# Kernel optimization log

Measured on AMD Instinct MI355X. Metric: run time of the kernel, lower is better.

Reference implementation:

```python
import jax, jax.numpy as jnp
import numpy as np

T, B, F_, H = 128, 64, 512, 1024  # time, batch, feat, hidden


def hamilton(w):
    """Build dense quaternion (Hamilton-product) weight matrix.
    w: (4, in//4, out//4) components (r, i, j, k) -> (in, out)."""
    r, i, j, k = w[0], w[1], w[2], w[3]
    return jnp.concatenate([
        jnp.concatenate([r, -i, -j, -k], axis=0),
        jnp.concatenate([i,  r, -k,  j], axis=0),
        jnp.concatenate([j,  k,  r, -i], axis=0),
        jnp.concatenate([k, -j,  i,  r], axis=0),
    ], axis=1)


def setup_inputs() -> dict:
    key = jax.random.key(0)
    ks = jax.random.split(key, 16)
    s_in, s_h = 0.05, 0.03  # small init scales for stable gates
    d = {"x": jax.random.normal(ks[0], (T, B, F_), jnp.float32)}
    for idx, n in enumerate(["wfx", "wix", "wox", "wcx"]):
        d[n + "_w"] = jax.random.normal(ks[1 + idx], (4, F_ // 4, H // 4), jnp.float32) * s_in
        d[n + "_b"] = jnp.zeros((H,), jnp.float32)
    for idx, n in enumerate(["ufh", "uih", "uoh", "uch"]):
        d[n + "_w"] = jax.random.normal(ks[5 + idx], (4, H // 4, H // 4), jnp.float32) * s_h
    d["fco_w"] = jax.random.normal(ks[9], (H, F_ + 1), jnp.float32) * 0.02
    d["fco_b"] = jnp.zeros((F_ + 1,), jnp.float32)
    return d


def reference(x, wfx_w, wfx_b, wix_w, wix_b, wox_w, wox_b, wcx_w, wcx_b,
              ufh_w, uih_w, uoh_w, uch_w, fco_w, fco_b):
    # Dense quaternion matrices built once (as torch does per call).
    Wf, Wi, Wo, Wc = (hamilton(w) for w in (wfx_w, wix_w, wox_w, wcx_w))
    Uf, Ui, Uo, Uc = (hamilton(w) for w in (ufh_w, uih_w, uoh_w, uch_w))
    # Precompute all input projections over the whole sequence (as torch does).
    gf = jnp.einsum('tbi,io->tbo', x, Wf) + wfx_b
    gi = jnp.einsum('tbi,io->tbo', x, Wi) + wix_b
    go = jnp.einsum('tbi,io->tbo', x, Wo) + wox_b
    gc = jnp.einsum('tbi,io->tbo', x, Wc) + wcx_b

    def step(carry, g):
        h, c = carry
        gft, git, got, gct = g
        ft = jax.nn.sigmoid(gft + h @ Uf)
        it = jax.nn.sigmoid(git + h @ Ui)
        ot = jax.nn.sigmoid(got + h @ Uo)
        at = gct + h @ Uc
        c = it * jnp.tanh(at) + ft * c
        h = ot * jnp.tanh(c)
        return (h, c), h @ fco_w + fco_b

    h0 = jnp.zeros((B, H), x.dtype)
    _, out = jax.lax.scan(step, (h0, h0), (gf, gi, go, gc))
    return out  # [T, B, F_+1]
```

## Files before the change

### kernel.cpp

```cpp
#include <hip/hip_runtime.h>
#include <stdint.h>

typedef _Float16 f16;
typedef _Float16 f16x8 __attribute__((ext_vector_type(8)));
typedef short bf16x8 __attribute__((ext_vector_type(8)));
typedef float f32x4 __attribute__((ext_vector_type(4)));

#define H_ 1024
#define NG_ 4096
#define F_ 512
#define B_ 64
#define T_ 128
#define NOP_ 640
#define NO_ 513
#define NBLK_R 128

__constant__ int c_comp[16] = {0,1,2,3, 1,0,3,2, 2,3,0,1, 3,2,1,0};
__constant__ float c_sgnf[16] = {1,1,1,1, -1,1,1,-1, -1,-1,1,1, -1,1,-1,1};

__device__ __forceinline__ float bf2f(unsigned short u){
  union { unsigned int i; float f; } v; v.i = ((unsigned int)u) << 16; return v.f;
}
__device__ __forceinline__ unsigned short f2bf(float f){
  union { float f; unsigned int i; } v; v.f = f;
  return (unsigned short)((v.i + 0x7fffu + ((v.i >> 16) & 1u)) >> 16);
}
__device__ __forceinline__ float ldin(const void* p, int i, int f){
  return f ? ((const float*)p)[i] : bf2f(((const unsigned short*)p)[i]);
}
__device__ __forceinline__ float sigm(float x){ return 1.f / (1.f + __expf(-x)); }
__device__ __forceinline__ float tanh_(float x){
  float ax = fabsf(x);
  float e = __expf(-2.f * ax);
  float t = (1.f - e) / (1.f + e);
  return x < 0.f ? -t : t;
}

__device__ __forceinline__ void load_a8_nw(const f16* p, f16x8* a){
  asm volatile(
    "global_load_dwordx4 %0, %8, off sc0 sc1\n\t"
    "global_load_dwordx4 %1, %8, off offset:64 sc0 sc1\n\t"
    "global_load_dwordx4 %2, %8, off offset:128 sc0 sc1\n\t"
    "global_load_dwordx4 %3, %8, off offset:192 sc0 sc1\n\t"
    "global_load_dwordx4 %4, %8, off offset:256 sc0 sc1\n\t"
    "global_load_dwordx4 %5, %8, off offset:320 sc0 sc1\n\t"
    "global_load_dwordx4 %6, %8, off offset:384 sc0 sc1\n\t"
    "global_load_dwordx4 %7, %8, off offset:448 sc0 sc1"
    : "=&v"(a[0]),"=&v"(a[1]),"=&v"(a[2]),"=&v"(a[3]),
      "=&v"(a[4]),"=&v"(a[5]),"=&v"(a[6]),"=&v"(a[7])
    : "v"(p) : "memory");
}
__device__ __forceinline__ void load_c8(const unsigned short* p, bf16x8* a){
  asm volatile(
    "global_load_dwordx4 %0, %8, off\n\t"
    "global_load_dwordx4 %1, %8, off offset:64\n\t"
    "global_load_dwordx4 %2, %8, off offset:128\n\t"
    "global_load_dwordx4 %3, %8, off offset:192\n\t"
    "global_load_dwordx4 %4, %8, off offset:256\n\t"
    "global_load_dwordx4 %5, %8, off offset:320\n\t"
    "global_load_dwordx4 %6, %8, off offset:384\n\t"
    "global_load_dwordx4 %7, %8, off offset:448"
    : "=&v"(a[0]),"=&v"(a[1]),"=&v"(a[2]),"=&v"(a[3]),
      "=&v"(a[4]),"=&v"(a[5]),"=&v"(a[6]),"=&v"(a[7])
    : "v"(p) : "memory");
}
__device__ __forceinline__ void store_h_sys(f16* p, f16 v){
  asm volatile("global_store_short %0, %1, off sc0 sc1" :: "v"(p), "v"(v) : "memory");
}
__device__ __forceinline__ void store_flag_sys(int* p, int v){
  asm volatile("global_store_dword %0, %1, off sc0 sc1" :: "v"(p), "v"(v) : "memory");
}
__device__ __forceinline__ void load_flag2_sys(const int* p0, const int* p1, int &a, int &b){
  asm volatile(
    "global_load_dword %0, %2, off sc0 sc1\n\t"
    "global_load_dword %1, %3, off sc0 sc1\n\t"
    "s_waitcnt vmcnt(0)"
    : "=&v"(a), "=&v"(b) : "v"(p0), "v"(p1) : "memory");
}
__device__ __forceinline__ void drain_vmem(){
  asm volatile("s_waitcnt vmcnt(0)" ::: "memory");
}
#define WAIT_VM(n) do { \
  asm volatile("s_waitcnt vmcnt(" #n ")" ::: "memory"); \
  __builtin_amdgcn_sched_barrier(0); \
} while (0)

#define WX_ELEMS (NG_*F_)
#define U_ELEMS  (NG_*H_)
#define FCO_ELEMS (NOP_*H_)
#define BIAS_ELEMS NG_
#define OB_ELEMS NOP_
#define XC_ELEMS (T_*B_*F_)
#define HZ_ELEMS (B_*H_)
#define FZ_ELEMS (NBLK_R*16)
#define PACK_TOTAL (WX_ELEMS + U_ELEMS + FCO_ELEMS + BIAS_ELEMS + OB_ELEMS + XC_ELEMS + HZ_ELEMS + FZ_ELEMS)

__global__ void pack_kernel(
    const void* __restrict__ x,
    const void* __restrict__ wf, const void* __restrict__ wi,
    const void* __restrict__ wo, const void* __restrict__ wc,
    const void* __restrict__ bfv, const void* __restrict__ biv,
    const void* __restrict__ bov, const void* __restrict__ bcv,
    const void* __restrict__ uf, const void* __restrict__ ui,
    const void* __restrict__ uo, const void* __restrict__ uc,
    const void* __restrict__ fcw, const void* __restrict__ fcb,
    unsigned short* __restrict__ Wx, f16* __restrict__ U, f16* __restrict__ Fco,
    float* __restrict__ bias, float* __restrict__ ob,
    unsigned short* __restrict__ Xc,
    f16* __restrict__ Hz, int* __restrict__ Fz)
{
  __shared__ int zc, wc2;
  if (threadIdx.x == 0){ zc = 0; wc2 = 0; }
  __syncthreads();
  {
    const unsigned short* xu = (const unsigned short*)x;
    unsigned short u = xu[2 * threadIdx.x];
    int e = (u >> 7) & 0xFF;
    bool z = (u & 0x7FFF) == 0;
    bool wild = !z && (e < 67 || e > 150);
    if (z) atomicAdd(&zc, 1);
    if (wild) atomicAdd(&wc2, 1);
  }
  __syncthreads();
  const int fl = (zc >= 128 || wc2 >= 64) ? 1 : 0;

  int i = blockIdx.x * blockDim.x + threadIdx.x;
  if (i < WX_ELEMS) {
    int n = i >> 9, k = i & 511;
    int g = n >> 10, nn = n & 1023;
    int q = nn >> 8, be = nn & 255;
    int p = k >> 7, al = k & 127;
    const void* w = (g==0) ? wf : (g==1) ? wi : (g==2) ? wo : wc;
    int pq = p*4 + q;
    Wx[i] = f2bf(c_sgnf[pq] * ldin(w, c_comp[pq]*32768 + al*256 + be, fl));
    return;
  }
  i -= WX_ELEMS;
  if (i < U_ELEMS) {
    int n = i >> 10, k = i & 1023;
    int g = n >> 10;
    int q = (n & 1023) >> 8, be = n & 255;
    int p = k >> 8, al = k & 255;
    const void* u = (g==0) ? uf : (g==1) ? ui : (g==2) ? uo : uc;
    int pq = p*4 + q;
    U[i] = (f16)(c_sgnf[pq] * ldin(u, c_comp[pq]*65536 + al*256 + be, fl));
    return;
  }
  i -= U_ELEMS;
  if (i < FCO_ELEMS) {
    int n = i >> 10, k = i & 1023;
    Fco[i] = (n < NO_) ? (f16)ldin(fcw, k*NO_ + n, fl) : (f16)0.f;
    return;
  }
  i -= FCO_ELEMS;
  if (i < BIAS_ELEMS) {
    int g = i >> 10;
    const void* b = (g==0) ? bfv : (g==1) ? biv : (g==2) ? bov : bcv;
    bias[i] = ldin(b, i & 1023, fl);
    return;
  }
  i -= BIAS_ELEMS;
  if (i < OB_ELEMS) {
    ob[i] = (i < NO_) ? ldin(fcb, i, fl) : 0.f;
    return;
  }
  i -= OB_ELEMS;
  if (i < XC_ELEMS) {
    Xc[i] = fl ? f2bf(((const float*)x)[i]) : ((const unsigned short*)x)[i];
    return;
  }
  i -= XC_ELEMS;
  if (i < HZ_ELEMS) { Hz[i] = (f16)0.f; return; }
  i -= HZ_ELEMS;
  if (i < FZ_ELEMS) { Fz[i] = 0; }
}

__global__ __launch_bounds__(256) void recur_all(
    const unsigned short* __restrict__ Xc,
    const unsigned short* __restrict__ Wxp,
    const f16* __restrict__ U,
    const float* __restrict__ bias,
    f16* __restrict__ Hall,
    int* __restrict__ flags)
{
  __shared__ f16 Usm[32768];
  __shared__ unsigned short Wxsm[16384];
  const int blk = blockIdx.x;
  const int jb = blk * 8;
  const int tid = threadIdx.x;
  const int lane = tid & 63, w = tid >> 6;
  const int lo = lane & 15, quad = lane >> 4;
  const int m0 = w * 16;

  #pragma unroll
  for (int j = 0; j < 16; j++) {
    int u = tid + j*256;
    int lp = u & 63, f = u >> 6;
    int ki = f >> 1, nt = f & 1;
    int n = nt*16 + (lp & 15), qd = lp >> 4;
    int row = (n >> 3)*H_ + jb + (n & 7);
    *(f16x8*)(Usm + f*512 + lp*8) =
        *(const f16x8*)(U + (size_t)row*H_ + ki*32 + qd*8);
  }
  #pragma unroll
  for (int j = 0; j < 8; j++) {
    int u = tid + j*256;
    int lp = u & 63, f = u >> 6;
    int ku = f >> 1, p = f & 1;
    int col = (p*2 + ((lp & 15) >> 3))*1024 + jb + (lp & 7);
    *(f16x8*)((f16*)Wxsm + f*512 + lp*8) =
        *(const f16x8*)((const f16*)Wxp + (size_t)col*F_ + ku*32 + (lp >> 4)*8);
  }
  const int cc = lane & 7, hi = (lane >> 3) & 1;
  const int colg = jb + cc;
  const int b0r = m0 + quad*4 + hi*2;
  float creg[2] = {0.f, 0.f};
  const float bf0 = bias[colg];
  const float bf1 = bias[1024 + colg];
  const float bf2 = bias[2048 + colg];
  const float bf3 = bias[3072 + colg];
  __syncthreads();

  f32x4 xp0 = {0.f,0.f,0.f,0.f}, xp1 = {0.f,0.f,0.f,0.f};
  bf16x8 xa0[8], xa1[8];
  {
    const unsigned short* xr = Xc + (size_t)(m0 + lo)*F_ + quad*8;
    load_c8(xr, xa0);
    load_c8(xr + 256, xa1);
    drain_vmem();
    __builtin_amdgcn_sched_barrier(0);
    #pragma unroll
    for (int u = 0; u < 8; u++) {
      xp0 = __builtin_amdgcn_mfma_f32_16x16x32_bf16(xa0[u], *(const bf16x8*)((f16*)Wxsm + (u*2+0)*512 + lane*8), xp0, 0, 0, 0);
      xp1 = __builtin_amdgcn_mfma_f32_16x16x32_bf16(xa0[u], *(const bf16x8*)((f16*)Wxsm + (u*2+1)*512 + lane*8), xp1, 0, 0, 0);
    }
    #pragma unroll
    for (int u = 0; u < 8; u++) {
      xp0 = __builtin_amdgcn_mfma_f32_16x16x32_bf16(xa1[u], *(const bf16x8*)((f16*)Wxsm + ((8+u)*2+0)*512 + lane*8), xp0, 0, 0, 0);
      xp1 = __builtin_amdgcn_mfma_f32_16x16x32_bf16(xa1[u], *(const bf16x8*)((f16*)Wxsm + ((8+u)*2+1)*512 + lane*8), xp1, 0, 0, 0);
    }
  }

  for (int t = 0; t < T_; t++) {
    f32x4 acc0 = xp0, acc1 = xp1;
    const f16* Ap = Hall + (size_t)t*B_*H_ + (size_t)(m0 + lo)*H_ + quad*8;
    f16x8 a0[8], a1[8], a2[8], a3[8];
    drain_vmem();
    load_a8_nw(Ap,       a0);
    load_a8_nw(Ap + 256, a1);
    load_a8_nw(Ap + 512, a2);
    load_a8_nw(Ap + 768, a3);
    {
      const int tn = (t + 1 < T_) ? t + 1 : 0;
      const unsigned short* xr = Xc + (size_t)tn*B_*F_ + (size_t)(m0 + lo)*F_ + quad*8;
      load_c8(xr, xa0);
      load_c8(xr + 256, xa1);
    }
    WAIT_VM(40);
    #pragma unroll
    for (int u = 0; u < 8; u++) {
      f16x8 bb0 = *(const f16x8*)(Usm + ((u)*2+0)*512 + lane*8);
      f16x8 bb1 = *(const f16x8*)(Usm + ((u)*2+1)*512 + lane*8);
      acc0 = __builtin_amdgcn_mfma_f32_16x16x32_f16(a0[u], bb0, acc0, 0, 0, 0);
      acc1 = __builtin_amdgcn_mfma_f32_16x16x32_f16(a0[u], bb1, acc1, 0, 0, 0);
    }
    WAIT_VM(32);
    #pragma unroll
    for (int u = 0; u < 8; u++) {
      f16x8 bb0 = *(const f16x8*)(Usm + ((8+u)*2+0)*512 + lane*8);
      f16x8 bb1 = *(const f16x8*)(Usm + ((8+u)*2+1)*512 + lane*8);
      acc0 = __builtin_amdgcn_mfma_f32_16x16x32_f16(a1[u], bb0, acc0, 0, 0, 0);
      acc1 = __builtin_amdgcn_mfma_f32_16x16x32_f16(a1[u], bb1, acc1, 0, 0, 0);
    }
    WAIT_VM(24);
    #pragma unroll
    for (int u = 0; u < 8; u++) {
      f16x8 bb0 = *(const f16x8*)(Usm + ((16+u)*2+0)*512 + lane*8);
      f16x8 bb1 = *(const f16x8*)(Usm + ((16+u)*2+1)*512 + lane*8);
      acc0 = __builtin_amdgcn_mfma_f32_16x16x32_f16(a2[u], bb0, acc0, 0, 0, 0);
      acc1 = __builtin_amdgcn_mfma_f32_16x16x32_f16(a2[u], bb1, acc1, 0, 0, 0);
    }
    WAIT_VM(16);
    #pragma unroll
    for (int u = 0; u < 8; u++) {
      f16x8 bb0 = *(const f16x8*)(Usm + ((24+u)*2+0)*512 + lane*8);
      f16x8 bb1 = *(const f16x8*)(Usm + ((24+u)*2+1)*512 + lane*8);
      acc0 = __builtin_amdgcn_mfma_f32_16x16x32_f16(a3[u], bb0, acc0, 0, 0, 0);
      acc1 = __builtin_amdgcn_mfma_f32_16x16x32_f16(a3[u], bb1, acc1, 0, 0, 0);
    }
    WAIT_VM(0);
    f16* Hn = Hall + (size_t)(t+1)*B_*H_;
    #pragma unroll
    for (int e = 0; e < 2; e++) {
      int src = quad*16 + cc;
      float f_lo = __shfl(acc0[e],   src);
      float f_hi = __shfl(acc0[2+e], src);
      float i_lo = __shfl(acc0[e],   src + 8);
      float i_hi = __shfl(acc0[2+e], src + 8);
      float o_lo = __shfl(acc1[e],   src);
      float o_hi = __shfl(acc1[2+e], src);
      float a_lo = __shfl(acc1[e],   src + 8);
      float a_hi = __shfl(acc1[2+e], src + 8);
      float pf = (hi ? f_hi : f_lo) + bf0;
      float pi = (hi ? i_hi : i_lo) + bf1;
      float po = (hi ? o_hi : o_lo) + bf2;
      float pa = (hi ? a_hi : a_lo) + bf3;
      float vf = sigm(pf), vi = sigm(pi), vo = sigm(po);
      creg[e] = vi * tanh_(pa) + vf * creg[e];
      float hn = vo * tanh_(creg[e]);
      store_h_sys(Hn + (size_t)(b0r + e)*H_ + colg, (f16)hn);
    }
    if (t + 1 < T_) {
      drain_vmem();
      __syncthreads();
      const int target = t + 1;
      if (tid == 0) store_flag_sys(flags + blk*16, target);
      xp0 = (f32x4){0.f,0.f,0.f,0.f};
      xp1 = (f32x4){0.f,0.f,0.f,0.f};
      #pragma unroll
      for (int u = 0; u < 8; u++) {
        xp0 = __builtin_amdgcn_mfma_f32_16x16x32_bf16(xa0[u], *(const bf16x8*)((f16*)Wxsm + (u*2+0)*512 + lane*8), xp0, 0, 0, 0);
        xp1 = __builtin_amdgcn_mfma_f32_16x16x32_bf16(xa0[u], *(const bf16x8*)((f16*)Wxsm + (u*2+1)*512 + lane*8), xp1, 0, 0, 0);
      }
      #pragma unroll
      for (int u = 0; u < 8; u++) {
        xp0 = __builtin_amdgcn_mfma_f32_16x16x32_bf16(xa1[u], *(const bf16x8*)((f16*)Wxsm + ((8+u)*2+0)*512 + lane*8), xp0, 0, 0, 0);
        xp1 = __builtin_amdgcn_mfma_f32_16x16x32_bf16(xa1[u], *(const bf16x8*)((f16*)Wxsm + ((8+u)*2+1)*512 + lane*8), xp1, 0, 0, 0);
      }
      __builtin_amdgcn_sched_barrier(0);
      if (w == 0) {
        const int* fp0 = flags + (2*lane)*16;
        const int* fp1 = flags + (2*lane+1)*16;
        int f0, f1;
        do {
          load_flag2_sys(fp0, fp1, f0, f1);
        } while (!__all(f0 >= target && f1 >= target));
      }
      __syncthreads();
    } else {
      drain_vmem();
    }
  }
}

__global__ __launch_bounds__(256) void gemm_out(
    const f16* __restrict__ A,
    const f16* __restrict__ Bt,
    const float* __restrict__ ob,
    float* __restrict__ out)
{
  const int lane = threadIdx.x & 63, w = threadIdx.x >> 6;
  const int lo = lane & 15, quad = lane >> 4;
  const int m0 = blockIdx.x * 128 + (w >> 1) * 64;
  const int n0 = blockIdx.y * 128 + (w & 1) * 64;
  f32x4 acc[4][4] = {};
  #pragma unroll 2
  for (int k0 = 0; k0 < H_; k0 += 32) {
    f16x8 a[4], b[4];
    #pragma unroll
    for (int mt = 0; mt < 4; mt++)
      a[mt] = *(const f16x8*)(A + (size_t)(m0 + 16*mt + lo) * H_ + k0 + quad*8);
    #pragma unroll
    for (int nt = 0; nt < 4; nt++)
      b[nt] = *(const f16x8*)(Bt + (size_t)(n0 + 16*nt + lo) * H_ + k0 + quad*8);
    #pragma unroll
    for (int mt = 0; mt < 4; mt++)
      #pragma unroll
      for (int nt = 0; nt < 4; nt++)
        acc[mt][nt] = __builtin_amdgcn_mfma_f32_16x16x32_f16(a[mt], b[nt], acc[mt][nt], 0, 0, 0);
  }
  #pragma unroll
  for (int mt = 0; mt < 4; mt++)
    #pragma unroll
    for (int nt = 0; nt < 4; nt++)
      #pragma unroll
      for (int r = 0; r < 4; r++) {
        int row = m0 + 16*mt + quad*4 + r;
        int col = n0 + 16*nt + lo;
        if (col < NO_)
          out[(size_t)row * NO_ + col] = acc[mt][nt][r] + ob[col];
      }
}

extern "C" void kernel_launch(void* const* d_in, const int* in_sizes, int n_in,
                              void* d_out, int out_size, void* d_ws, size_t ws_size,
                              hipStream_t stream)
{
  const void* x   = d_in[0];
  const void* wfw = d_in[1];  const void* wfb = d_in[2];
  const void* wiw = d_in[3];  const void* wib = d_in[4];
  const void* wow = d_in[5];  const void* wob = d_in[6];
  const void* wcw = d_in[7];  const void* wcb = d_in[8];
  const void* ufw = d_in[9];  const void* uiw = d_in[10];
  const void* uow = d_in[11]; const void* ucw = d_in[12];
  const void* fcw = d_in[13]; const void* fcb = d_in[14];

  char* ws = (char*)d_ws;
  unsigned short* Wx = (unsigned short*)(ws + 0);
  f16*   U    = (f16*)  (ws + 4194304);
  f16*   Fco  = (f16*)  (ws + 12582912);
  unsigned short* Xc = (unsigned short*)(ws + 13893632);
  f16*   Hall = (f16*)  (ws + 22282240);
  float* bias = (float*)(ws + 39190528);
  float* ob   = (float*)(ws + 39206912);
  int*   flags= (int*)  (ws + 39209472);
  if (ws_size < 39217664u) return;

  pack_kernel<<<(PACK_TOTAL + 255)/256, 256, 0, stream>>>(
      x, wfw, wiw, wow, wcw, wfb, wib, wob, wcb, ufw, uiw, uow, ucw, fcw, fcb,
      Wx, U, Fco, bias, ob, Xc, Hall, flags);

  {
    const unsigned short* Xcp = Xc;
    const unsigned short* Wxp = Wx;
    const f16* Up = U;
    const float* bp = bias;
    f16* Hp = Hall;
    int* flp = flags;
    void* args[] = {&Xcp, &Wxp, &Up, &bp, &Hp, &flp};
    hipLaunchCooperativeKernel((const void*)recur_all, dim3(NBLK_R), dim3(256),
                               args, 0, stream);
  }

  gemm_out<<<dim3(64, 5), 256, 0, stream>>>(Hall + (size_t)B_*H_, Fco, ob, (float*)d_out);
}
```

Measured before the change: 1.165 ms.

## Halve recurrent grid to 64 blocks of 512 threads, stream Wx from global

The persistent recurrent kernel now runs 64 cooperative blocks of 512 threads, each covering 16 hidden columns with two column groups of waves. This halves the number of blocks that must be polled at every timestep barrier. U slices for both column groups go into shared memory, which grows to 128 KB. To make room, the input-projection weights are no longer held in LDS and are reloaded from global/L2 into registers every step, adding memory traffic and a full drain on the critical path.

```diff
diff --git a/kernel.cpp b/kernel.cpp
--- a/kernel.cpp
+++ b/kernel.cpp
@@ -13,7 +13,7 @@
 #define T_ 128
 #define NOP_ 640
 #define NO_ 513
-#define NBLK_R 128
+#define NBLK_R 64
 
 __constant__ int c_comp[16] = {0,1,2,3, 1,0,3,2, 2,3,0,1, 3,2,1,0};
 __constant__ float c_sgnf[16] = {1,1,1,1, -1,1,1,-1, -1,-1,1,1, -1,1,-1,1};
@@ -70,12 +70,11 @@
 __device__ __forceinline__ void store_flag_sys(int* p, int v){
   asm volatile("global_store_dword %0, %1, off sc0 sc1" :: "v"(p), "v"(v) : "memory");
 }
-__device__ __forceinline__ void load_flag2_sys(const int* p0, const int* p1, int &a, int &b){
+__device__ __forceinline__ void load_flag1_sys(const int* p, int &a){
   asm volatile(
-    "global_load_dword %0, %2, off sc0 sc1\n\t"
-    "global_load_dword %1, %3, off sc0 sc1\n\t"
+    "global_load_dword %0, %1, off sc0 sc1\n\t"
     "s_waitcnt vmcnt(0)"
-    : "=&v"(a), "=&v"(b) : "v"(p0), "v"(p1) : "memory");
+    : "=&v"(a) : "v"(p) : "memory");
 }
 __device__ __forceinline__ void drain_vmem(){
   asm volatile("s_waitcnt vmcnt(0)" ::: "memory");
@@ -175,7 +174,7 @@
   if (i < FZ_ELEMS) { Fz[i] = 0; }
 }
 
-__global__ __launch_bounds__(256) void recur_all(
+__global__ __launch_bounds__(512, 2) void recur_all(
     const unsigned short* __restrict__ Xc,
     const unsigned short* __restrict__ Wxp,
     const f16* __restrict__ U,
@@ -183,61 +182,64 @@
     f16* __restrict__ Hall,
     int* __restrict__ flags)
 {
-  __shared__ f16 Usm[32768];
-  __shared__ unsigned short Wxsm[16384];
+  __shared__ f16 Usm[65536];
   const int blk = blockIdx.x;
-  const int jb = blk * 8;
+  const int jb = blk * 16;
   const int tid = threadIdx.x;
   const int lane = tid & 63, w = tid >> 6;
+  const int cg = w & 1, rg = w >> 1;
   const int lo = lane & 15, quad = lane >> 4;
-  const int m0 = w * 16;
+  const int m0 = rg * 16;
+  const int jbc = jb + cg * 8;
 
   #pragma unroll
   for (int j = 0; j < 16; j++) {
-    int u = tid + j*256;
-    int lp = u & 63, f = u >> 6;
+    int u = tid + j*512;
+    int cgs = u >> 12;
+    int uu = u & 4095;
+    int lp = uu & 63, f = uu >> 6;
     int ki = f >> 1, nt = f & 1;
     int n = nt*16 + (lp & 15), qd = lp >> 4;
-    int row = (n >> 3)*H_ + jb + (n & 7);
-    *(f16x8*)(Usm + f*512 + lp*8) =
+    int row = (n >> 3)*H_ + jb + cgs*8 + (n & 7);
+    *(f16x8*)(Usm + cgs*32768 + f*512 + lp*8) =
         *(const f16x8*)(U + (size_t)row*H_ + ki*32 + qd*8);
   }
-  #pragma unroll
-  for (int j = 0; j < 8; j++) {
-    int u = tid + j*256;
-    int lp = u & 63, f = u >> 6;
-    int ku = f >> 1, p = f & 1;
-    int col = (p*2 + ((lp & 15) >> 3))*1024 + jb + (lp & 7);
-    *(f16x8*)((f16*)Wxsm + f*512 + lp*8) =
-        *(const f16x8*)((const f16*)Wxp + (size_t)col*F_ + ku*32 + (lp >> 4)*8);
-  }
+  const f16* Us = Usm + cg*32768;
   const int cc = lane & 7, hi = (lane >> 3) & 1;
-  const int colg = jb + cc;
+  const int colg = jbc + cc;
   const int b0r = m0 + quad*4 + hi*2;
   float creg[2] = {0.f, 0.f};
   const float bf0 = bias[colg];
   const float bf1 = bias[1024 + colg];
   const float bf2 = bias[2048 + colg];
   const float bf3 = bias[3072 + colg];
+  const unsigned short* wxb0 = Wxp + (size_t)((lo >> 3)*1024 + jbc + (lo & 7))*F_ + quad*8;
+  const unsigned short* wxb1 = Wxp + (size_t)((2 + (lo >> 3))*1024 + jbc + (lo & 7))*F_ + quad*8;
   __syncthreads();
 
   f32x4 xp0 = {0.f,0.f,0.f,0.f}, xp1 = {0.f,0.f,0.f,0.f};
-  bf16x8 xa0[8], xa1[8];
+  bf16x8 xa0[8], xa1[8], xb0[8], xb1[8];
   {
     const unsigned short* xr = Xc + (size_t)(m0 + lo)*F_ + quad*8;
     load_c8(xr, xa0);
     load_c8(xr + 256, xa1);
+    load_c8(wxb0, xb0);
+    load_c8(wxb1, xb1);
     drain_vmem();
     __builtin_amdgcn_sched_barrier(0);
     #pragma unroll
     for (int u = 0; u < 8; u++) {
-      xp0 = __builtin_amdgcn_mfma_f32_16x16x32_bf16(xa0[u], *(const bf16x8*)((f16*)Wxsm + (u*2+0)*512 + lane*8), xp0, 0, 0, 0);
-      xp1 = __builtin_amdgcn_mfma_f32_16x16x32_bf16(xa0[u], *(const bf16x8*)((f16*)Wxsm + (u*2+1)*512 + lane*8), xp1, 0, 0, 0);
-    }
-    #pragma unroll
-    for (int u = 0; u < 8; u++) {
-      xp0 = __builtin_amdgcn_mfma_f32_16x16x32_bf16(xa1[u], *(const bf16x8*)((f16*)Wxsm + ((8+u)*2+0)*512 + lane*8), xp0, 0, 0, 0);
-      xp1 = __builtin_amdgcn_mfma_f32_16x16x32_bf16(xa1[u], *(const bf16x8*)((f16*)Wxsm + ((8+u)*2+1)*512 + lane*8), xp1, 0, 0, 0);
+      xp0 = __builtin_amdgcn_mfma_f32_16x16x32_bf16(xa0[u], xb0[u], xp0, 0, 0, 0);
+      xp1 = __builtin_amdgcn_mfma_f32_16x16x32_bf16(xa0[u], xb1[u], xp1, 0, 0, 0);
+    }
+    load_c8(wxb0 + 256, xb0);
+    load_c8(wxb1 + 256, xb1);
+    drain_vmem();
+    __builtin_amdgcn_sched_barrier(0);
+    #pragma unroll
+    for (int u = 0; u < 8; u++) {
+      xp0 = __builtin_amdgcn_mfma_f32_16x16x32_bf16(xa1[u], xb0[u], xp0, 0, 0, 0);
+      xp1 = __builtin_amdgcn_mfma_f32_16x16x32_bf16(xa1[u], xb1[u], xp1, 0, 0, 0);
     }
   }
 
@@ -259,32 +261,32 @@
     WAIT_VM(40);
     #pragma unroll
     for (int u = 0; u < 8; u++) {
-      f16x8 bb0 = *(const f16x8*)(Usm + ((u)*2+0)*512 + lane*8);
-      f16x8 bb1 = *(const f16x8*)(Usm + ((u)*2+1)*512 + lane*8);
+      f16x8 bb0 = *(const f16x8*)(Us + ((u)*2+0)*512 + lane*8);
+      f16x8 bb1 = *(const f16x8*)(Us + ((u)*2+1)*512 + lane*8);
       acc0 = __builtin_amdgcn_mfma_f32_16x16x32_f16(a0[u], bb0, acc0, 0, 0, 0);
       acc1 = __builtin_amdgcn_mfma_f32_16x16x32_f16(a0[u], bb1, acc1, 0, 0, 0);
     }
     WAIT_VM(32);
     #pragma unroll
     for (int u = 0; u < 8; u++) {
-      f16x8 bb0 = *(const f16x8*)(Usm + ((8+u)*2+0)*512 + lane*8);
-      f16x8 bb1 = *(const f16x8*)(Usm + ((8+u)*2+1)*512 + lane*8);
+      f16x8 bb0 = *(const f16x8*)(Us + ((8+u)*2+0)*512 + lane*8);
+      f16x8 bb1 = *(const f16x8*)(Us + ((8+u)*2+1)*512 + lane*8);
       acc0 = __builtin_amdgcn_mfma_f32_16x16x32_f16(a1[u], bb0, acc0, 0, 0, 0);
       acc1 = __builtin_amdgcn_mfma_f32_16x16x32_f16(a1[u], bb1, acc1, 0, 0, 0);
     }
     WAIT_VM(24);
     #pragma unroll
     for (int u = 0; u < 8; u++) {
-      f16x8 bb0 = *(const f16x8*)(Usm + ((16+u)*2+0)*512 + lane*8);
-      f16x8 bb1 = *(const f16x8*)(Usm + ((16+u)*2+1)*512 + lane*8);
+      f16x8 bb0 = *(const f16x8*)(Us + ((16+u)*2+0)*512 + lane*8);
+      f16x8 bb1 = *(const f16x8*)(Us + ((16+u)*2+1)*512 + lane*8);
       acc0 = __builtin_amdgcn_mfma_f32_16x16x32_f16(a2[u], bb0, acc0, 0, 0, 0);
       acc1 = __builtin_amdgcn_mfma_f32_16x16x32_f16(a2[u], bb1, acc1, 0, 0, 0);
     }
     WAIT_VM(16);
     #pragma unroll
     for (int u = 0; u < 8; u++) {
-      f16x8 bb0 = *(const f16x8*)(Usm + ((24+u)*2+0)*512 + lane*8);
-      f16x8 bb1 = *(const f16x8*)(Usm + ((24+u)*2+1)*512 + lane*8);
+      f16x8 bb0 = *(const f16x8*)(Us + ((24+u)*2+0)*512 + lane*8);
+      f16x8 bb1 = *(const f16x8*)(Us + ((24+u)*2+1)*512 + lane*8);
       acc0 = __builtin_amdgcn_mfma_f32_16x16x32_f16(a3[u], bb0, acc0, 0, 0, 0);
       acc1 = __builtin_amdgcn_mfma_f32_16x16x32_f16(a3[u], bb1, acc1, 0, 0, 0);
     }
@@ -317,24 +319,31 @@
       if (tid == 0) store_flag_sys(flags + blk*16, target);
       xp0 = (f32x4){0.f,0.f,0.f,0.f};
       xp1 = (f32x4){0.f,0.f,0.f,0.f};
+      load_c8(wxb0, xb0);
+      load_c8(wxb1, xb1);
+      drain_vmem();
+      __builtin_amdgcn_sched_barrier(0);
       #pragma unroll
       for (int u = 0; u < 8; u++) {
-        xp0 = __builtin_amdgcn_mfma_f32_16x16x32_bf16(xa0[u], *(const bf16x8*)((f16*)Wxsm + (u*2+0)*512 + lane*8), xp0, 0, 0, 0);
-        xp1 = __builtin_amdgcn_mfma_f32_16x16x32_bf16(xa0[u], *(const bf16x8*)((f16*)Wxsm + (u*2+1)*512 + lane*8), xp1, 0, 0, 0);
+        xp0 = __builtin_amdgcn_mfma_f32_16x16x32_bf16(xa0[u], xb0[u], xp0, 0, 0, 0);
+        xp1 = __builtin_amdgcn_mfma_f32_16x16x32_bf16(xa0[u], xb1[u], xp1, 0, 0, 0);
       }
+      load_c8(wxb0 + 256, xb0);
+      load_c8(wxb1 + 256, xb1);
+      drain_vmem();
+      __builtin_amdgcn_sched_barrier(0);
       #pragma unroll
       for (int u = 0; u < 8; u++) {
-        xp0 = __builtin_amdgcn_mfma_f32_16x16x32_bf16(xa1[u], *(const bf16x8*)((f16*)Wxsm + ((8+u)*2+0)*512 + lane*8), xp0, 0, 0, 0);
-        xp1 = __builtin_amdgcn_mfma_f32_16x16x32_bf16(xa1[u], *(const bf16x8*)((f16*)Wxsm + ((8+u)*2+1)*512 + lane*8), xp1, 0, 0, 0);
+        xp0 = __builtin_amdgcn_mfma_f32_16x16x32_bf16(xa1[u], xb0[u], xp0, 0, 0, 0);
+        xp1 = __builtin_amdgcn_mfma_f32_16x16x32_bf16(xa1[u], xb1[u], xp1, 0, 0, 0);
       }
       __builtin_amdgcn_sched_barrier(0);
       if (w == 0) {
-        const int* fp0 = flags + (2*lane)*16;
-        const int* fp1 = flags + (2*lane+1)*16;
-        int f0, f1;
+        const int* fp = flags + lane*16;
+        int f0;
         do {
-          load_flag2_sys(fp0, fp1, f0, f1);
-        } while (!__all(f0 >= target && f1 >= target));
+          load_flag1_sys(fp, f0);
+        } while (!__all(f0 >= target));
       }
       __syncthreads();
     } else {
@@ -404,7 +413,7 @@
   float* bias = (float*)(ws + 39190528);
   float* ob   = (float*)(ws + 39206912);
   int*   flags= (int*)  (ws + 39209472);
-  if (ws_size < 39217664u) return;
+  if (ws_size < 39213568u) return;
 
   pack_kernel<<<(PACK_TOTAL + 255)/256, 256, 0, stream>>>(
       x, wfw, wiw, wow, wcw, wfb, wib, wob, wcb, ufw, uiw, uow, ucw, fcw, fcb,
@@ -418,7 +427,7 @@
     f16* Hp = Hall;
     int* flp = flags;
     void* args[] = {&Xcp, &Wxp, &Up, &bp, &Hp, &flp};
-    hipLaunchCooperativeKernel((const void*)recur_all, dim3(NBLK_R), dim3(256),
+    hipLaunchCooperativeKernel((const void*)recur_all, dim3(NBLK_R), dim3(512),
                                args, 0, stream);
   }
 
```

After: 2.630 ms. +125.8%, slower.
